# Kernel tuning notes

Hardware: AMD Instinct MI355X
Metric: run time of the kernel (lower is better)

Reference implementation:

```python
import jax, jax.numpy as jnp
import numpy as np

B, SQ, SK, D = 8, 512, 512, 32


def _spd_cov(key, b, s, d):
    # random SPD covariance: A A^T + I
    a = 0.1 * jax.random.normal(key, (b, s, d, d), dtype=jnp.float32)
    return jnp.einsum('bsde,bsfe->bsdf', a, a) + jnp.eye(d, dtype=jnp.float32)


def setup_inputs() -> dict:
    key = jax.random.key(0)
    ks = jax.random.split(key, 6)
    return {
        'q_mean': jax.random.normal(ks[0], (B, SQ, D), dtype=jnp.float32),
        'q_cov': _spd_cov(ks[1], B, SQ, D),
        'k_mean': jax.random.normal(ks[2], (B, SK, D), dtype=jnp.float32),
        'k_cov': _spd_cov(ks[3], B, SK, D),
        'v_mean': jax.random.normal(ks[4], (B, SK, D), dtype=jnp.float32),
        'v_cov': _spd_cov(ks[5], B, SK, D),
    }


def reference(q_mean, q_cov, k_mean, k_cov, v_mean, v_cov):
    # Pairwise symmetric Gaussian JSD attention.
    # JSD = 0.5*(KL(p_q||p_k)+KL(p_k||p_q)); the log-det terms cancel:
    # JSD = 0.25*( tr(Sk^-1 Sq) + tr(Sq^-1 Sk) - 2D
    #              + dm^T (Sk^-1 + Sq^-1) dm ),  dm = mu_q - mu_k
    d = q_mean.shape[-1]
    q_inv = jnp.linalg.inv(q_cov)            # [B,Sq,D,D]
    k_inv = jnp.linalg.inv(k_cov)            # [B,Sk,D,D]
    tr_kq = jnp.einsum('bkde,bqed->bqk', k_inv, q_cov)
    tr_qk = jnp.einsum('bqde,bked->bqk', q_inv, k_cov)
    dm = q_mean[:, :, None, :] - k_mean[:, None, :, :]   # [B,Sq,Sk,D]
    quad = (jnp.einsum('bqkd,bkde,bqke->bqk', dm, k_inv, dm)
            + jnp.einsum('bqkd,bqde,bqke->bqk', dm, q_inv, dm))
    js = 0.25 * (tr_kq + tr_qk - 2.0 * d + quad)         # [B,Sq,Sk]
    score = jax.nn.softmax(js, axis=-1)
    out_mean = jnp.einsum('bqk,bkd->bqd', score, v_mean)
    out_cov = jnp.einsum('bqk,bkde->bqde', score, v_cov)
    return out_mean, out_cov
```

## Files before the change

kernel.cpp:

```cpp
#include <hip/hip_runtime.h>
#include <hip/hip_bf16.h>

#define NBATCH 8
#define SQL 512
#define SKL 512
#define DD 32
#define KF 1152
#define UT 528
#define NOUT 1056
#define NVT 1088
#define NSITE (NBATCH * SQL)
#define FEAT_BLOCKS (2 * NSITE / 8)
#define VS_BLOCKS (34 * 16 * NBATCH)

typedef short short8 __attribute__((ext_vector_type(8)));
typedef float f32x4 __attribute__((ext_vector_type(4)));
typedef unsigned short ushort_t;

__device__ __forceinline__ ushort_t f2bf(float f) {
    unsigned int u = __float_as_uint(f);
    return (ushort_t)((u + 0x7fffu + ((u >> 16) & 1u)) >> 16);
}
__device__ __forceinline__ float bf2f(ushort_t h) {
    return __uint_as_float(((unsigned int)h) << 16);
}
__device__ __forceinline__ void gl_lds16(const ushort_t* g, ushort_t* l) {
    __builtin_amdgcn_global_load_lds(
        (const __attribute__((address_space(1))) void*)g,
        (__attribute__((address_space(3))) void*)l, 16, 0, 0);
}
__device__ __forceinline__ void pk_split(float v0, float v1, ushort_t& h0, ushort_t& h1,
                                         ushort_t& l0, ushort_t& l1) {
    __hip_bfloat162 H = __float22bfloat162_rn(make_float2(v0, v1));
    ushort2 hu = *(ushort2*)&H;
    h0 = hu.x; h1 = hu.y;
    __hip_bfloat162 L = __float22bfloat162_rn(make_float2(v0 - bf2f(hu.x), v1 - bf2f(hu.y)));
    ushort2 lu = *(ushort2*)&L;
    l0 = lu.x; l1 = lu.y;
}

template<int P>
__device__ __forceinline__ float swzb(float x) {
    return __int_as_float(__builtin_amdgcn_ds_swizzle(__float_as_int(x), (P << 5)));
}
template<int M>
__device__ __forceinline__ float swzx(float x) {
    return __int_as_float(__builtin_amdgcn_ds_swizzle(__float_as_int(x), (M << 10) | 0x1F));
}

template<int P>
__device__ __forceinline__ void gj_step(float (&a)[DD], int hl) {
    float piv = swzb<P>(a[P]);
    float rinv = __builtin_amdgcn_rcpf(piv);
    float t = a[P] * rinv;
    bool isp = (hl == P);
    float u = isp ? rinv : t;
    float g = isp ? 0.0f : 1.0f;
    #pragma unroll
    for (int i = 0; i < DD; ++i) {
        if (i == P) continue;
        float ci = swzb<P>(a[i]);
        a[i] = fmaf(a[i], g, -(ci * u));
    }
    a[P] = u;
}
template<int P>
__device__ __forceinline__ void gj_run(float (&a)[DD], int hl) {
    gj_step<P>(a, hl);
    if constexpr (P + 1 < DD) gj_run<P + 1>(a, hl);
}

__global__ __launch_bounds__(256, 4) void feat_kernel(
    const float* __restrict__ qm, const float* __restrict__ qc,
    const float* __restrict__ km, const float* __restrict__ kc,
    ushort_t* __restrict__ fqh, ushort_t* __restrict__ fql,
    ushort_t* __restrict__ fkh, ushort_t* __restrict__ fkl)
{
    __shared__ float smem[8 * 1064 + 8 * 32];
    const int tid = threadIdx.x;
    const int wid = tid >> 6, lane = tid & 63;
    const int half = lane >> 5, hl = lane & 31;
    const int site_g = (blockIdx.x * 4 + wid) * 2 + half;
    const int qside = site_g < NSITE;
    const int site = qside ? site_g : site_g - NSITE;

    const float* covp = (qside ? qc : kc) + (size_t)site * (DD * DD);
    const float* mup  = (qside ? qm : km) + (size_t)site * DD;
    ushort_t* fh = qside ? fqh : fkh;
    ushort_t* fl = qside ? fql : fkl;
    const size_t fo = (size_t)site * KF;

    float* inv_s = smem + (wid * 2 + half) * 1064;
    float* mu_s  = smem + 8 * 1064 + (wid * 2 + half) * 32;

    const float mu_lane = mup[hl];
    mu_s[hl] = mu_lane;

    float a[DD];
    #pragma unroll
    for (int r = 0; r < DD; ++r) a[r] = covp[r * DD + hl];

    gj_run<0>(a, hl);

    #pragma unroll
    for (int r = 0; r < DD; ++r) inv_s[r * 33 + hl] = a[r];

    float ivr = 0.f;
    #pragma unroll
    for (int e = 0; e < DD; ++e) ivr = fmaf(a[e], mu_s[e], ivr);

    float pb = mu_lane * ivr;
    pb += swzx<1>(pb); pb += swzx<2>(pb); pb += swzx<4>(pb);
    pb += swzx<8>(pb); pb += swzx<16>(pb);
    const float bias = pb;

    for (int idx = hl; idx < UT; idx += 32) {
        int d = (int)((65.0f - sqrtf(4225.0f - 8.0f * (float)idx)) * 0.5f);
        if (d > 0 && (d * (65 - d)) / 2 > idx) --d;
        if (((d + 1) * (64 - d)) / 2 <= idx) ++d;
        int off = (d * (65 - d)) / 2;
        int e = d + (idx - off);
        float Mv = covp[d * DD + e] + mu_s[d] * mu_s[e];
        float Iv = inv_s[d * 33 + e];
        float w = (d == e) ? 0.25f : 0.5f;
        float v0, v1;
        if (qside) { v0 = w * Mv; v1 = w * Iv; }
        else       { v0 = Iv;     v1 = Mv; }
        ushort_t h0, h1, l0, l1;
        pk_split(v0, v1, h0, h1, l0, l1);
        fh[fo + idx] = h0; fh[fo + UT + idx] = h1;
        fl[fo + idx] = l0; fl[fo + UT + idx] = l1;
    }
    {
        float v0, v1;
        if (qside) { v0 = -0.5f * ivr; v1 = 0.25f * mu_lane; }
        else       { v0 = mu_lane;     v1 = -2.f * ivr; }
        ushort_t h0, h1, l0, l1;
        pk_split(v0, v1, h0, h1, l0, l1);
        fh[fo + 2*UT + hl] = h0; fh[fo + 2*UT + DD + hl] = h1;
        fl[fo + 2*UT + hl] = l0; fl[fo + 2*UT + DD + hl] = l1;
    }
    if (hl == 0) {
        float v = qside ? 0.25f : bias;
        ushort_t hb = f2bf(v);
        fh[fo + 2*UT + 2*DD] = hb;
        fl[fo + 2*UT + 2*DD] = f2bf(v - bf2f(hb));
    }
    for (int i = 2*UT + 2*DD + 1 + hl; i < KF; i += 32) { fh[fo + i] = 0; fl[fo + i] = 0; }
}

__global__ __launch_bounds__(256) void vt_kernel(
    const float* __restrict__ vmean, const float* __restrict__ vcov,
    ushort_t* __restrict__ vth)
{
    __shared__ float sm[32 * 33];
    const int tid = threadIdx.x;
    const int vb = blockIdx.x;
    const int b = vb / (34 * 16), rem = vb % (34 * 16);
    const int kt = rem / 34, nt = rem % 34;
    const int n0 = nt * 32, k0 = kt * 32;
    const int tx = tid & 31, ty = tid >> 5;
    for (int r = ty; r < 32; r += 8) {
        const int k = k0 + r, n = n0 + tx;
        float v;
        if (n0 == 0)          v = vmean[((size_t)b * SKL + k) * DD + n];
        else if (n0 >= NOUT)  v = 0.f;
        else                  v = vcov[((size_t)b * SKL + k) * (DD * DD) + (n - DD)];
        sm[tx * 33 + r] = v;
    }
    __syncthreads();
    for (int r = ty; r < 32; r += 8) {
        const int n = n0 + r, k = k0 + tx;
        vth[((size_t)b * NVT + n) * SKL + k] = f2bf(sm[r * 33 + tx]);
    }
}

template<int MODE, int DUAL>
__global__ __launch_bounds__(256) void gemm_split(
    const ushort_t* __restrict__ Ah_g, const ushort_t* __restrict__ Al_g,
    const ushort_t* __restrict__ Bh_g, const ushort_t* __restrict__ Bl_g,
    float* __restrict__ C0, float* __restrict__ C1)
{
    constexpr bool SPLIT = (MODE == 0);
    constexpr int KSTRIDE = SPLIT ? KF : SKL;
    constexpr int KITERS = SPLIT ? (KF / 2 / 32) : (SKL / 32);
    const int b = blockIdx.z, nt = blockIdx.x;
    const int mt = SPLIT ? (blockIdx.y & 3) : blockIdx.y;
    const int ks = SPLIT ? (blockIdx.y >> 2) : 0;
    const int kbase = ks * (SPLIT ? (KF / 2) : 0);
    const int tid = threadIdx.x, lane = tid & 63, wid = tid >> 6;
    const int wm = wid & 1, wn = wid >> 1;
    const int BROWS = MODE ? NVT : SKL;

    const ushort_t* Ah = Ah_g + ((size_t)b * SQL + mt * 128) * KSTRIDE;
    const ushort_t* Al = Al_g + ((size_t)b * SQL + mt * 128) * KSTRIDE;
    const ushort_t* Bh = Bh_g + ((size_t)b * BROWS + nt * 64) * KSTRIDE;
    const ushort_t* Bl = Bl_g + ((size_t)b * BROWS + nt * 64) * KSTRIDE;

    __shared__ __align__(16) ushort_t AsH[128 * 32];
    __shared__ __align__(16) ushort_t AsL[SPLIT ? 128 * 32 : 8];
    __shared__ __align__(16) ushort_t BsH[64 * 32];
    __shared__ __align__(16) ushort_t BsL[SPLIT ? 64 * 32 : 8];

    const int r4 = lane >> 2, kp = (lane & 3) * 8;
    const int arow0 = wid * 16 + r4,        aoff0 = wid * 512 + lane * 8;
    const int arow1 = (wid + 4) * 16 + r4,  aoff1 = (wid + 4) * 512 + lane * 8;

    const int fm = lane & 15;
    const int q8 = (lane >> 4) * 8;

    f32x4 acc[4][2];
    #pragma unroll
    for (int i = 0; i < 4; ++i)
        #pragma unroll
        for (int j = 0; j < 2; ++j)
            acc[i][j] = (f32x4){0.f, 0.f, 0.f, 0.f};

    for (int it = 0; it < KITERS; ++it) {
        const int k0 = kbase + it * 32;
        __syncthreads();
        gl_lds16(Ah + (size_t)arow0 * KSTRIDE + k0 + kp, &AsH[aoff0]);
        gl_lds16(Ah + (size_t)arow1 * KSTRIDE + k0 + kp, &AsH[aoff1]);
        gl_lds16(Bh + (size_t)arow0 * KSTRIDE + k0 + kp, &BsH[aoff0]);
        if (SPLIT) {
            gl_lds16(Al + (size_t)arow0 * KSTRIDE + k0 + kp, &AsL[aoff0]);
            gl_lds16(Al + (size_t)arow1 * KSTRIDE + k0 + kp, &AsL[aoff1]);
            gl_lds16(Bl + (size_t)arow0 * KSTRIDE + k0 + kp, &BsL[aoff0]);
        }
        __syncthreads();

        short8 ah[4], al[4], bh[2], bl[2];
        #pragma unroll
        for (int i = 0; i < 4; ++i) {
            const int r = wm * 64 + i * 16 + fm;
            ah[i] = *(const short8*)&AsH[r * 32 + q8];
            if (SPLIT) al[i] = *(const short8*)&AsL[r * 32 + q8];
        }
        #pragma unroll
        for (int j = 0; j < 2; ++j) {
            const int r = wn * 32 + j * 16 + fm;
            bh[j] = *(const short8*)&BsH[r * 32 + q8];
            if (SPLIT) bl[j] = *(const short8*)&BsL[r * 32 + q8];
        }
        #pragma unroll
        for (int i = 0; i < 4; ++i)
            #pragma unroll
            for (int j = 0; j < 2; ++j) {
                acc[i][j] = __builtin_amdgcn_mfma_f32_16x16x32_bf16(ah[i], bh[j], acc[i][j], 0, 0, 0);
                if (SPLIT) {
                    acc[i][j] = __builtin_amdgcn_mfma_f32_16x16x32_bf16(ah[i], bl[j], acc[i][j], 0, 0, 0);
                    acc[i][j] = __builtin_amdgcn_mfma_f32_16x16x32_bf16(al[i], bh[j], acc[i][j], 0, 0, 0);
                }
            }
    }

    float* Cs = (SPLIT && DUAL && ks) ? C1 : C0;
    const int crow0 = (lane >> 4) * 4;
    const int ccol = lane & 15;
    #pragma unroll
    for (int i = 0; i < 4; ++i) {
        const int m = mt * 128 + wm * 64 + i * 16 + crow0;
        #pragma unroll
        for (int j = 0; j < 2; ++j) {
            const int n = nt * 64 + wn * 32 + j * 16 + ccol;
            #pragma unroll
            for (int r = 0; r < 4; ++r) {
                const float v = acc[i][j][r];
                const size_t rowb = (size_t)b * SQL + (m + r);
                if (MODE == 0) {
                    if (DUAL) Cs[rowb * SKL + n] = v;
                    else      atomicAdd(&C0[rowb * SKL + n], v);
                } else {
                    if (n < DD)        C0[rowb * DD + n] = v;
                    else if (n < NOUT) C1[rowb * (DD * DD) + (n - DD)] = v;
                }
            }
        }
    }
}

template<int DUAL>
__global__ __launch_bounds__(256) void softmax_rows(
    const float* __restrict__ js0, const float* __restrict__ js1,
    ushort_t* __restrict__ ph)
{
    __shared__ float sm[8];
    const int tid = threadIdx.x;
    const size_t ro = (size_t)blockIdx.x * SKL + 2 * tid;
    float2 v = *(const float2*)(js0 + ro);
    if (DUAL) {
        float2 v1 = *(const float2*)(js1 + ro);
        v.x += v1.x; v.y += v1.y;
    }
    float m = fmaxf(v.x, v.y);
    #pragma unroll
    for (int o = 32; o > 0; o >>= 1) m = fmaxf(m, __shfl_xor(m, o));
    const int wid = tid >> 6, ln = tid & 63;
    if (ln == 0) sm[wid] = m;
    __syncthreads();
    m = fmaxf(fmaxf(sm[0], sm[1]), fmaxf(sm[2], sm[3]));
    float e0 = __expf(v.x - m), e1 = __expf(v.y - m);
    float s = e0 + e1;
    #pragma unroll
    for (int o = 32; o > 0; o >>= 1) s += __shfl_xor(s, o);
    if (ln == 0) sm[4 + wid] = s;
    __syncthreads();
    s = sm[4] + sm[5] + sm[6] + sm[7];
    float rs = 1.0f / s;
    ph[ro]     = f2bf(e0 * rs);
    ph[ro + 1] = f2bf(e1 * rs);
}

extern "C" void kernel_launch(void* const* d_in, const int* in_sizes, int n_in,
                              void* d_out, int out_size, void* d_ws, size_t ws_size,
                              hipStream_t stream)
{
    const float* q_mean = (const float*)d_in[0];
    const float* q_cov  = (const float*)d_in[1];
    const float* k_mean = (const float*)d_in[2];
    const float* k_cov  = (const float*)d_in[3];
    const float* v_mean = (const float*)d_in[4];
    const float* v_cov  = (const float*)d_in[5];

    float* out_mean = (float*)d_out;
    float* out_cov  = out_mean + (size_t)NBATCH * SQL * DD;

    char* w = (char*)d_ws;
    const size_t FQN = (size_t)NBATCH * SQL * KF;
    const size_t JSN = (size_t)NBATCH * SQL * SKL;
    const size_t VTN = (size_t)NBATCH * NVT * SKL;
    ushort_t* fq_h = (ushort_t*)w;
    ushort_t* fq_l = fq_h + FQN;
    ushort_t* fk_h = fq_l + FQN;
    ushort_t* fk_l = fk_h + FQN;
    float*    js0  = (float*)(fk_l + FQN);
    const bool dual = ws_size >= (8 * FQN + 8 * JSN + 2 * VTN);
    float*    js1  = dual ? (js0 + JSN) : nullptr;
    ushort_t* vt_h = (ushort_t*)(js0 + (dual ? 2 : 1) * JSN);
    ushort_t* p_h  = fk_h;

    feat_kernel<<<FEAT_BLOCKS, 256, 0, stream>>>(
        q_mean, q_cov, k_mean, k_cov, fq_h, fq_l, fk_h, fk_l);
    vt_kernel<<<VS_BLOCKS, 256, 0, stream>>>(v_mean, v_cov, vt_h);
    if (dual) {
        gemm_split<0, 1><<<dim3(SKL / 64, 8, NBATCH), 256, 0, stream>>>(
            fq_h, fq_l, fk_h, fk_l, js0, js1);
        softmax_rows<1><<<NBATCH * SQL, 256, 0, stream>>>(js0, js1, p_h);
    } else {
        hipMemsetAsync(js0, 0, JSN * sizeof(float), stream);
        gemm_split<0, 0><<<dim3(SKL / 64, 8, NBATCH), 256, 0, stream>>>(
            fq_h, fq_l, fk_h, fk_l, js0, nullptr);
        softmax_rows<0><<<NBATCH * SQL, 256, 0, stream>>>(js0, nullptr, p_h);
    }
    gemm_split<1, 0><<<dim3(NVT / 64, SQL / 128, NBATCH), 256, 0, stream>>>(
        p_h, nullptr, vt_h, nullptr, out_mean, out_cov);
}
```

Before: 182.9 us.

## Invert four matrices per wavefront with two columns per lane in feat_kernel

Gauss-Jordan inversion in feat_kernel now gives each lane two columns held as float2, so one 64-lane wave works on four 32x32 matrices instead of two. Pivot broadcasts use a different ds_swizzle pattern over 16-lane groups. Each block now covers 16 sites, so the grid is halved and per-block LDS and registers roughly double; launch bounds drop to 2 blocks per CU. This cuts the number of swizzle broadcasts per matrix and raises per-lane ILP, at the cost of higher register pressure and lower occupancy.

```diff
diff --git a/kernel.cpp b/kernel.cpp
--- a/kernel.cpp
+++ b/kernel.cpp
@@ -10,7 +10,7 @@
 #define NOUT 1056
 #define NVT 1088
 #define NSITE (NBATCH * SQL)
-#define FEAT_BLOCKS (2 * NSITE / 8)
+#define FEAT_BLOCKS (2 * NSITE / 16)
 #define VS_BLOCKS (34 * 16 * NBATCH)
 
 typedef short short8 __attribute__((ext_vector_type(8)));
@@ -40,8 +40,9 @@
 }
 
 template<int P>
-__device__ __forceinline__ float swzb(float x) {
-    return __int_as_float(__builtin_amdgcn_ds_swizzle(__float_as_int(x), (P << 5)));
+__device__ __forceinline__ float swzg(float x) {
+    return __int_as_float(__builtin_amdgcn_ds_swizzle(
+        __float_as_int(x), ((P >> 1) << 5) | 0x10));
 }
 template<int M>
 __device__ __forceinline__ float swzx(float x) {
@@ -49,38 +50,40 @@
 }
 
 template<int P>
-__device__ __forceinline__ void gj_step(float (&a)[DD], int hl) {
-    float piv = swzb<P>(a[P]);
-    float rinv = __builtin_amdgcn_rcpf(piv);
-    float t = a[P] * rinv;
-    bool isp = (hl == P);
-    float u = isp ? rinv : t;
-    float g = isp ? 0.0f : 1.0f;
+__device__ __forceinline__ void gj_step4(float2 (&a)[DD], int s2) {
+    float dpv = swzg<P>((P & 1) ? a[P].y : a[P].x);
+    float rinv = __builtin_amdgcn_rcpf(dpv);
+    const bool isp0 = (s2 == P), isp1 = (s2 + 1 == P);
+    float2 u, g;
+    u.x = isp0 ? rinv : a[P].x * rinv;  g.x = isp0 ? 0.f : 1.f;
+    u.y = isp1 ? rinv : a[P].y * rinv;  g.y = isp1 ? 0.f : 1.f;
     #pragma unroll
     for (int i = 0; i < DD; ++i) {
         if (i == P) continue;
-        float ci = swzb<P>(a[i]);
-        a[i] = fmaf(a[i], g, -(ci * u));
+        float ci = swzg<P>((P & 1) ? a[i].y : a[i].x);
+        a[i].x = fmaf(a[i].x, g.x, -(ci * u.x));
+        a[i].y = fmaf(a[i].y, g.y, -(ci * u.y));
     }
     a[P] = u;
 }
 template<int P>
-__device__ __forceinline__ void gj_run(float (&a)[DD], int hl) {
-    gj_step<P>(a, hl);
-    if constexpr (P + 1 < DD) gj_run<P + 1>(a, hl);
-}
-
-__global__ __launch_bounds__(256, 4) void feat_kernel(
+__device__ __forceinline__ void gj_run4(float2 (&a)[DD], int s2) {
+    gj_step4<P>(a, s2);
+    if constexpr (P + 1 < DD) gj_run4<P + 1>(a, s2);
+}
+
+__global__ __launch_bounds__(256, 2) void feat_kernel(
     const float* __restrict__ qm, const float* __restrict__ qc,
     const float* __restrict__ km, const float* __restrict__ kc,
     ushort_t* __restrict__ fqh, ushort_t* __restrict__ fql,
     ushort_t* __restrict__ fkh, ushort_t* __restrict__ fkl)
 {
-    __shared__ float smem[8 * 1064 + 8 * 32];
+    __shared__ float smem[16 * 1088 + 16 * 32];
     const int tid = threadIdx.x;
     const int wid = tid >> 6, lane = tid & 63;
-    const int half = lane >> 5, hl = lane & 31;
-    const int site_g = (blockIdx.x * 4 + wid) * 2 + half;
+    const int grp = lane >> 4, s = lane & 15, s2 = s * 2;
+    const int mtx = wid * 4 + grp;
+    const int site_g = blockIdx.x * 16 + mtx;
     const int qside = site_g < NSITE;
     const int site = qside ? site_g : site_g - NSITE;
 
@@ -90,38 +93,41 @@
     ushort_t* fl = qside ? fql : fkl;
     const size_t fo = (size_t)site * KF;
 
-    float* inv_s = smem + (wid * 2 + half) * 1064;
-    float* mu_s  = smem + 8 * 1064 + (wid * 2 + half) * 32;
-
-    const float mu_lane = mup[hl];
-    mu_s[hl] = mu_lane;
-
-    float a[DD];
-    #pragma unroll
-    for (int r = 0; r < DD; ++r) a[r] = covp[r * DD + hl];
-
-    gj_run<0>(a, hl);
-
-    #pragma unroll
-    for (int r = 0; r < DD; ++r) inv_s[r * 33 + hl] = a[r];
-
-    float ivr = 0.f;
-    #pragma unroll
-    for (int e = 0; e < DD; ++e) ivr = fmaf(a[e], mu_s[e], ivr);
-
-    float pb = mu_lane * ivr;
-    pb += swzx<1>(pb); pb += swzx<2>(pb); pb += swzx<4>(pb);
-    pb += swzx<8>(pb); pb += swzx<16>(pb);
+    float* inv_s = smem + mtx * 1088;
+    float* mu_s  = smem + 16 * 1088 + mtx * 32;
+
+    const float2 mu2 = *(const float2*)(mup + s2);
+    *(float2*)(mu_s + s2) = mu2;
+
+    float2 a[DD];
+    #pragma unroll
+    for (int r = 0; r < DD; ++r) a[r] = *(const float2*)(covp + r * DD + s2);
+
+    gj_run4<0>(a, s2);
+
+    #pragma unroll
+    for (int r = 0; r < DD; ++r) *(float2*)(inv_s + r * 34 + s2) = a[r];
+
+    float ivr0 = 0.f, ivr1 = 0.f;
+    #pragma unroll
+    for (int e = 0; e < DD; ++e) {
+        float me = mu_s[e];
+        ivr0 = fmaf(a[e].x, me, ivr0);
+        ivr1 = fmaf(a[e].y, me, ivr1);
+    }
+
+    float pb = mu2.x * ivr0 + mu2.y * ivr1;
+    pb += swzx<1>(pb); pb += swzx<2>(pb); pb += swzx<4>(pb); pb += swzx<8>(pb);
     const float bias = pb;
 
-    for (int idx = hl; idx < UT; idx += 32) {
+    for (int idx = s; idx < UT; idx += 16) {
         int d = (int)((65.0f - sqrtf(4225.0f - 8.0f * (float)idx)) * 0.5f);
         if (d > 0 && (d * (65 - d)) / 2 > idx) --d;
         if (((d + 1) * (64 - d)) / 2 <= idx) ++d;
         int off = (d * (65 - d)) / 2;
         int e = d + (idx - off);
         float Mv = covp[d * DD + e] + mu_s[d] * mu_s[e];
-        float Iv = inv_s[d * 33 + e];
+        float Iv = inv_s[d * 34 + e];
         float w = (d == e) ? 0.25f : 0.5f;
         float v0, v1;
         if (qside) { v0 = w * Mv; v1 = w * Iv; }
@@ -132,21 +138,26 @@
         fl[fo + idx] = l0; fl[fo + UT + idx] = l1;
     }
     {
-        float v0, v1;
-        if (qside) { v0 = -0.5f * ivr; v1 = 0.25f * mu_lane; }
-        else       { v0 = mu_lane;     v1 = -2.f * ivr; }
-        ushort_t h0, h1, l0, l1;
-        pk_split(v0, v1, h0, h1, l0, l1);
-        fh[fo + 2*UT + hl] = h0; fh[fo + 2*UT + DD + hl] = h1;
-        fl[fo + 2*UT + hl] = l0; fl[fo + 2*UT + DD + hl] = l1;
-    }
-    if (hl == 0) {
+        float iv[2] = {ivr0, ivr1}, mv[2] = {mu2.x, mu2.y};
+        #pragma unroll
+        for (int c = 0; c < 2; ++c) {
+            const int e = s2 + c;
+            float v0, v1;
+            if (qside) { v0 = -0.5f * iv[c]; v1 = 0.25f * mv[c]; }
+            else       { v0 = mv[c];         v1 = -2.f * iv[c]; }
+            ushort_t h0, h1, l0, l1;
+            pk_split(v0, v1, h0, h1, l0, l1);
+            fh[fo + 2*UT + e] = h0; fh[fo + 2*UT + DD + e] = h1;
+            fl[fo + 2*UT + e] = l0; fl[fo + 2*UT + DD + e] = l1;
+        }
+    }
+    if (s == 0) {
         float v = qside ? 0.25f : bias;
         ushort_t hb = f2bf(v);
         fh[fo + 2*UT + 2*DD] = hb;
         fl[fo + 2*UT + 2*DD] = f2bf(v - bf2f(hb));
     }
-    for (int i = 2*UT + 2*DD + 1 + hl; i < KF; i += 32) { fh[fo + i] = 0; fl[fo + i] = 0; }
+    for (int i = 2*UT + 2*DD + 1 + s; i < KF; i += 16) { fh[fo + i] = 0; fl[fo + i] = 0; }
 }
 
 __global__ __launch_bounds__(256) void vt_kernel(
```

After: 187.6 us. +2.6%, slower.
